# Kernel optimization log

Measured on AMD Instinct MI355X. Metric: run time of the kernel, lower is better.

The kernel has to match this reference:

```python
import jax, jax.numpy as jnp
import numpy as np

B, H, W, C, NH = 400, 14, 14, 768, 12
HD = C // NH  # 64


def setup_inputs() -> dict:
    key = jax.random.key(0)
    ks = jax.random.split(key, 6)
    s = 0.02
    return {
        "hidden_states": jax.random.normal(ks[0], (B, H, W, C), jnp.float32),
        "qkv_w": jax.random.normal(ks[1], (3 * C, C), jnp.float32) * s,
        "qkv_b": jnp.zeros((3 * C,), jnp.float32),
        "proj_w": jax.random.normal(ks[2], (C, C), jnp.float32) * s,
        "proj_b": jnp.zeros((C,), jnp.float32),
        "rel_pos_h": jax.random.normal(ks[3], (2 * H - 1, HD), jnp.float32) * s,
        "rel_pos_w": jax.random.normal(ks[4], (2 * W - 1, HD), jnp.float32) * s,
    }


def _get_rel_pos(q_size, k_size, rel_pos):
    # q_size == k_size and table already has 2*k-1 entries -> pure gather,
    # matching SamVisionAttention.get_rel_pos without interpolation.
    coords = jnp.arange(q_size)[:, None] - jnp.arange(k_size)[None, :] + (k_size - 1)
    return rel_pos[coords]  # (q, k, head_dim)


def reference(hidden_states, qkv_w, qkv_b, proj_w, proj_b, rel_pos_h, rel_pos_w):
    b, h, w, c = hidden_states.shape
    scale = HD ** -0.5
    # qkv projection: (b, h*w, 3c) -> (3, b, nh, hw, hd)
    qkv = hidden_states.reshape(b, h * w, c) @ qkv_w.T + qkv_b
    qkv = qkv.reshape(b, h * w, 3, NH, HD).transpose(2, 0, 3, 1, 4)
    q, k, v = qkv[0], qkv[1], qkv[2]
    # decomposed relative position bias (computed from UNSCALED q, as in SAM)
    Rh = _get_rel_pos(h, h, rel_pos_h)  # (h, h, hd)
    Rw = _get_rel_pos(w, w, rel_pos_w)  # (w, w, hd)
    qr = q.reshape(b, NH, h, w, HD)
    rel_h = jnp.einsum('bnhwc,hkc->bnhwk', qr, Rh)  # (b, nh, h, w, h)
    rel_w = jnp.einsum('bnhwc,wkc->bnhwk', qr, Rw)  # (b, nh, h, w, w)
    bias = (rel_h[..., :, None] + rel_w[..., None, :]).reshape(b, NH, h * w, h * w)
    # attention
    attn = jnp.einsum('bnqd,bnkd->bnqk', q, k) * scale + bias
    attn = jax.nn.softmax(attn, axis=-1)
    out = jnp.einsum('bnqk,bnkd->bnqd', attn, v)
    out = out.transpose(0, 2, 1, 3).reshape(b, h, w, c)
    return out @ proj_w.T + proj_b
```

## Files before the change

kernel.cpp:

```cpp
#include <hip/hip_runtime.h>
#include <hip/hip_bf16.h>

typedef __bf16 bfv8 __attribute__((ext_vector_type(8)));
typedef __bf16 bfv4 __attribute__((ext_vector_type(4)));
typedef float f32x4 __attribute__((ext_vector_type(4)));
typedef unsigned int u32x2 __attribute__((ext_vector_type(2)));
typedef unsigned short u16;
typedef unsigned int u32;

#define MT 78400

#define SBAR() __builtin_amdgcn_s_barrier()
#define VMCNT(n) asm volatile("s_waitcnt vmcnt(" #n ")" ::: "memory")

__device__ __forceinline__ u16 f2bf(float f) {
  u32 x = __float_as_uint(f);
  return (u16)((x + 0x7FFFu + ((x >> 16) & 1u)) >> 16);
}

__device__ __forceinline__ void gld16(const void* g, void* l) {
  __builtin_amdgcn_global_load_lds((const __attribute__((address_space(1))) void*)g,
                                   (__attribute__((address_space(3))) void*)l, 16, 0, 0);
}

__global__ __launch_bounds__(256) void cvt_f32_bf16(const float* __restrict__ src,
                                                    u16* __restrict__ dst, int n8) {
  int stride = gridDim.x * 256;
  for (int i = blockIdx.x * 256 + threadIdx.x; i < n8; i += stride) {
    const float4* s = (const float4*)(src + (long)i * 8);
    float4 a = s[0], b = s[1];
    u32 p0 = f2bf(a.x) | ((u32)f2bf(a.y) << 16);
    u32 p1 = f2bf(a.z) | ((u32)f2bf(a.w) << 16);
    u32 p2 = f2bf(b.x) | ((u32)f2bf(b.y) << 16);
    u32 p3 = f2bf(b.z) | ((u32)f2bf(b.w) << 16);
    uint4 o = {p0, p1, p2, p3};
    *(uint4*)(dst + (long)i * 8) = o;
  }
}

__global__ __launch_bounds__(256) void indk_init(u16* __restrict__ T) {
  int i = blockIdx.x * 256 + threadIdx.x;
  if (i < 208 * 40) {
    int k = i / 40, j = i - (i / 40) * 40;
    int hk = k / 14, wk = k - hk * 14;
    T[i] = (j == hk || j == 16 + wk) ? 0x3F80 : 0;
  }
}

__device__ __forceinline__ void gemm256_main(const u16* __restrict__ A, const u16* __restrict__ W,
                                             u16* SH, int m0, int n0, int tid,
                                             f32x4 (&acc)[8][4]) {
  const int lane = tid & 63;
  const int q15 = lane & 15, g = lane >> 4;
  const int wid = tid >> 6;
  const int wm = wid >> 2, wn = wid & 3;
  const int x0 = (g ^ (q15 & 7)) << 3;
  const int arow0 = wm * 128 + q15;
  const int brow0 = wn * 64 + q15;

  const int r0 = tid >> 3;
  const int gc0 = ((tid & 7) ^ (r0 & 7)) << 3;
  int ra00 = m0 + r0;       if (ra00 > MT - 1) ra00 = MT - 1;
  int ra10 = m0 + 64 + r0;  if (ra10 > MT - 1) ra10 = MT - 1;
  int ra01 = m0 + 128 + r0; if (ra01 > MT - 1) ra01 = MT - 1;
  int ra11 = m0 + 192 + r0; if (ra11 > MT - 1) ra11 = MT - 1;
  const u16* aS00 = A + (long)ra00 * 768 + gc0;
  const u16* aS10 = A + (long)ra10 * 768 + gc0;
  const u16* aS01 = A + (long)ra01 * 768 + gc0;
  const u16* aS11 = A + (long)ra11 * 768 + gc0;
  const u16* bS00 = W + (long)(n0 + r0) * 768 + gc0;
  const u16* bS10 = W + (long)(n0 + 64 + r0) * 768 + gc0;
  const u16* bS01 = W + (long)(n0 + 128 + r0) * 768 + gc0;
  const u16* bS11 = W + (long)(n0 + 192 + r0) * 768 + gc0;
  u16* dA = SH + tid * 8;
  u16* dB = dA + 16384;

  auto STGA = [&](int sl, const u16* p0, const u16* p1, int hoff, int kt) {
    u16* d = dA + sl * 32768 + hoff;
    gld16(p0 + kt * 64, d);
    gld16(p1 + kt * 64, d + 4096);
  };
  auto STGB = [&](int sl, const u16* p0, const u16* p1, int hoff, int kt) {
    u16* d = dB + sl * 32768 + hoff;
    gld16(p0 + kt * 64, d);
    gld16(p1 + kt * 64, d + 4096);
  };

  bfv8 b0[4], b1[4];
  bfv8 aX0[2], aX1[2], aY0[2], aY1[2];

  STGB(0, bS00, bS10, 0, 0); STGB(0, bS01, bS11, 8192, 0);
  STGA(0, aS00, aS10, 0, 0); STGA(0, aS01, aS11, 8192, 0);
  STGB(1, bS00, bS10, 0, 1); STGB(1, bS01, bS11, 8192, 1);
  STGA(1, aS00, aS10, 0, 1);
  VMCNT(4);
  SBAR();
  {
    const u16* Sb = SH + 16384;
#pragma unroll
    for (int ni = 0; ni < 4; ++ni) {
      const u16* bp = Sb + (brow0 + ni * 16) * 64;
      b0[ni] = *(const bfv8*)(bp + x0);
      b1[ni] = *(const bfv8*)(bp + (x0 ^ 32));
    }
#pragma unroll
    for (int m2 = 0; m2 < 2; ++m2) {
      const u16* ap = SH + (arow0 + m2 * 16) * 64;
      aX0[m2] = *(const bfv8*)(ap + x0);
      aX1[m2] = *(const bfv8*)(ap + (x0 ^ 32));
    }
  }

  for (int u = 0; u < 12; ++u) {
    const int sl = u & 1;
    const u16* Sa = SH + sl * 32768;
    const u16* San = SH + (sl ^ 1) * 32768;
    const u16* Sbn = San + 16384;
    const int kn1 = (u + 1 < 12) ? u + 1 : 11;
    const int kn2 = (u + 2 < 12) ? u + 2 : 11;

    __builtin_amdgcn_s_setprio(1);
#pragma unroll
    for (int m2 = 0; m2 < 2; ++m2)
#pragma unroll
      for (int ni = 0; ni < 4; ++ni)
        acc[m2][ni] = __builtin_amdgcn_mfma_f32_16x16x32_bf16(aX0[m2], b0[ni], acc[m2][ni], 0, 0, 0);
#pragma unroll
    for (int m2 = 0; m2 < 2; ++m2)
#pragma unroll
      for (int ni = 0; ni < 4; ++ni)
        acc[m2][ni] = __builtin_amdgcn_mfma_f32_16x16x32_bf16(aX1[m2], b1[ni], acc[m2][ni], 0, 0, 0);
    __builtin_amdgcn_s_setprio(0);
    SBAR();
#pragma unroll
    for (int m2 = 0; m2 < 2; ++m2) {
      const u16* ap = Sa + (arow0 + (2 + m2) * 16) * 64;
      aY0[m2] = *(const bfv8*)(ap + x0);
      aY1[m2] = *(const bfv8*)(ap + (x0 ^ 32));
    }
    STGA(sl ^ 1, aS01, aS11, 8192, kn1);

    __builtin_amdgcn_s_setprio(1);
#pragma unroll
    for (int m2 = 0; m2 < 2; ++m2)
#pragma unroll
      for (int ni = 0; ni < 4; ++ni)
        acc[2 + m2][ni] = __builtin_amdgcn_mfma_f32_16x16x32_bf16(aY0[m2], b0[ni], acc[2 + m2][ni], 0, 0, 0);
#pragma unroll
    for (int m2 = 0; m2 < 2; ++m2)
#pragma unroll
      for (int ni = 0; ni < 4; ++ni)
        acc[2 + m2][ni] = __builtin_amdgcn_mfma_f32_16x16x32_bf16(aY1[m2], b1[ni], acc[2 + m2][ni], 0, 0, 0);
    __builtin_amdgcn_s_setprio(0);
    SBAR();
#pragma unroll
    for (int m2 = 0; m2 < 2; ++m2) {
      const u16* ap = Sa + (arow0 + (4 + m2) * 16) * 64;
      aX0[m2] = *(const bfv8*)(ap + x0);
      aX1[m2] = *(const bfv8*)(ap + (x0 ^ 32));
    }
    STGB(sl, bS00, bS10, 0, kn2);

    __builtin_amdgcn_s_setprio(1);
#pragma unroll
    for (int m2 = 0; m2 < 2; ++m2)
#pragma unroll
      for (int ni = 0; ni < 4; ++ni)
        acc[4 + m2][ni] = __builtin_amdgcn_mfma_f32_16x16x32_bf16(aX0[m2], b0[ni], acc[4 + m2][ni], 0, 0, 0);
#pragma unroll
    for (int m2 = 0; m2 < 2; ++m2)
#pragma unroll
      for (int ni = 0; ni < 4; ++ni)
        acc[4 + m2][ni] = __builtin_amdgcn_mfma_f32_16x16x32_bf16(aX1[m2], b1[ni], acc[4 + m2][ni], 0, 0, 0);
    __builtin_amdgcn_s_setprio(0);
    SBAR();
#pragma unroll
    for (int m2 = 0; m2 < 2; ++m2) {
      const u16* ap = Sa + (arow0 + (6 + m2) * 16) * 64;
      aY0[m2] = *(const bfv8*)(ap + x0);
      aY1[m2] = *(const bfv8*)(ap + (x0 ^ 32));
    }
    STGB(sl, bS01, bS11, 8192, kn2);

    __builtin_amdgcn_s_setprio(1);
#pragma unroll
    for (int m2 = 0; m2 < 2; ++m2)
#pragma unroll
      for (int ni = 0; ni < 4; ++ni)
        acc[6 + m2][ni] = __builtin_amdgcn_mfma_f32_16x16x32_bf16(aY0[m2], b0[ni], acc[6 + m2][ni], 0, 0, 0);
#pragma unroll
    for (int m2 = 0; m2 < 2; ++m2)
#pragma unroll
      for (int ni = 0; ni < 4; ++ni)
        acc[6 + m2][ni] = __builtin_amdgcn_mfma_f32_16x16x32_bf16(aY1[m2], b1[ni], acc[6 + m2][ni], 0, 0, 0);
    __builtin_amdgcn_s_setprio(0);
    VMCNT(4);
    SBAR();
    if (u < 11) {
#pragma unroll
      for (int ni = 0; ni < 4; ++ni) {
        const u16* bp = Sbn + (brow0 + ni * 16) * 64;
        b0[ni] = *(const bfv8*)(bp + x0);
        b1[ni] = *(const bfv8*)(bp + (x0 ^ 32));
      }
#pragma unroll
      for (int m2 = 0; m2 < 2; ++m2) {
        const u16* ap = San + (arow0 + m2 * 16) * 64;
        aX0[m2] = *(const bfv8*)(ap + x0);
        aX1[m2] = *(const bfv8*)(ap + (x0 ^ 32));
      }
    }
    STGA(sl, aS00, aS10, 0, kn2);
  }
  VMCNT(0);
}

__global__ __launch_bounds__(512, 2) void qkv_gemm(const u16* __restrict__ A, const u16* __restrict__ W,
                                                   const float* __restrict__ bias,
                                                   u16* __restrict__ Qo, u16* __restrict__ Ko,
                                                   u16* __restrict__ Vo) {
  extern __shared__ u16 SH[];
  const int tid = threadIdx.x;
  const int orig = blockIdx.x;
  const int xcd = orig & 7, ii = orig >> 3;
  const int wg = (xcd < 3 ? xcd * 346 : 1038 + (xcd - 3) * 345) + ii;
  const int mt = wg / 9, nt = wg - mt * 9;
  const int m0 = mt * 256, n0 = nt * 256;

  f32x4 acc[8][4];
#pragma unroll
  for (int i = 0; i < 8; ++i)
#pragma unroll
    for (int j = 0; j < 4; ++j) acc[i][j] = (f32x4){0.f, 0.f, 0.f, 0.f};

  gemm256_main(A, W, SH, m0, n0, tid, acc);

  const int lane = tid & 63, q15 = lane & 15, g = lane >> 4;
  const int wid = tid >> 6, wm = wid >> 2, wn = wid & 3;
  __syncthreads();
  const int sel = nt / 3;
  u16* dst = (sel == 0) ? Qo : (sel == 1) ? Ko : Vo;
  const int ntr = nt - sel * 3;
  u16* Cs = SH;

#pragma unroll
  for (int h = 0; h < 2; ++h) {
    if (wm == h) {
#pragma unroll
      for (int ni = 0; ni < 4; ++ni) {
        int col = wn * 64 + ni * 16 + q15;
        float bb = bias[n0 + col];
#pragma unroll
        for (int mi = 0; mi < 8; ++mi)
#pragma unroll
          for (int r = 0; r < 4; ++r)
            Cs[(mi * 16 + g * 4 + r) * 264 + col] = f2bf(acc[mi][ni][r] + bb);
      }
    }
    __syncthreads();
#pragma unroll
    for (int j = 0; j < 8; ++j) {
      int idx = tid + 512 * j;
      int row = idx >> 5, cc = idx & 31;
      int m = m0 + h * 128 + row;
      if (m < MT) {
        int b = m / 196, s = m - b * 196;
        int nh = ntr * 4 + (cc >> 3);
        int hd0 = (cc & 7) * 8;
        uint4 v = *(const uint4*)(Cs + row * 264 + cc * 8);
        *(uint4*)(dst + (long)b * 150528 + (long)s * 64 + nh * 12544 + hd0) = v;
      }
    }
    if (h == 0) __syncthreads();
  }
}

__global__ __launch_bounds__(512, 2) void proj_gemm(const u16* __restrict__ A, const u16* __restrict__ W,
                                                    const float* __restrict__ bias,
                                                    float* __restrict__ out) {
  extern __shared__ u16 SH[];
  const int tid = threadIdx.x;
  const int orig = blockIdx.x;
  const int xcd = orig & 7, ii = orig >> 3;
  const int wg = (xcd < 1 ? xcd * 116 : 116 + (xcd - 1) * 115) + ii;
  const int mt = wg / 3, nt = wg - mt * 3;
  const int m0 = mt * 256, n0 = nt * 256;

  f32x4 acc[8][4];
#pragma unroll
  for (int i = 0; i < 8; ++i)
#pragma unroll
    for (int j = 0; j < 4; ++j) acc[i][j] = (f32x4){0.f, 0.f, 0.f, 0.f};

  gemm256_main(A, W, SH, m0, n0, tid, acc);

  const int lane = tid & 63, q15 = lane & 15, g = lane >> 4;
  const int wid = tid >> 6, wm = wid >> 2, wn = wid & 3;

#pragma unroll
  for (int ni = 0; ni < 4; ++ni) {
    int n = n0 + wn * 64 + ni * 16 + q15;
    float bb = bias[n];
#pragma unroll
    for (int mi = 0; mi < 8; ++mi)
#pragma unroll
      for (int r = 0; r < 4; ++r) {
        int m = m0 + wm * 128 + mi * 16 + g * 4 + r;
        if (m < MT) out[(long)m * 768 + n] = acc[mi][ni][r] + bb;
      }
  }
}

#define KLDS_OFF 0
#define VT_OFF   26624
#define TH_OFF   59392
#define TW_OFF   63280
#define AW_OFF   67168
#define SMEM_SZ  77408

__global__ __launch_bounds__(512, 2) void attn_kernel(const u16* __restrict__ Q, const u16* __restrict__ K,
                                                      const u16* __restrict__ V,
                                                      const float* __restrict__ rph, const float* __restrict__ rpw,
                                                      const u16* __restrict__ IndKg,
                                                      u16* __restrict__ AO) {
  extern __shared__ char smem[];
  u16* Klds = (u16*)(smem + KLDS_OFF);
  u16* VT = (u16*)(smem + VT_OFF);
  u16* TH = (u16*)(smem + TH_OFF);
  u16* TW = (u16*)(smem + TW_OFF);
  const int tid = threadIdx.x, lane = tid & 63, wid = tid >> 6;
  const int q15 = lane & 15, g = lane >> 4;
  const int bnh = blockIdx.x;
  const int b = bnh / 12, nh = bnh - b * 12;
  const u16* Qg = Q + bnh * 12544;
  const u16* Kg = K + bnh * 12544;
  const u16* Vg = V + bnh * 12544;
  u16* AWw = (u16*)(smem + AW_OFF) + wid * 16 * 40;

  for (int c = tid; c < 1568; c += 512) {
    int krow = c >> 3, part = c & 7;
    gld16(Kg + krow * 64 + ((part ^ (krow & 7)) << 3), Klds + c * 8);
  }
  for (int idx = tid; idx < 1792; idx += 512) {
    int k = idx >> 3, nb = idx & 7;
    u32 w0 = 0, w1 = 0, w2 = 0, w3 = 0;
    if (k < 196) {
      uint4 t = *(const uint4*)(Vg + k * 64 + nb * 8);
      w0 = t.x; w1 = t.y; w2 = t.z; w3 = t.w;
    }
    u32 wv[4] = {w0, w1, w2, w3};
#pragma unroll
    for (int j = 0; j < 8; j++) {
      int n = nb * 8 + j;
      u16 val = (u16)(wv[j >> 1] >> ((j & 1) * 16));
      int blk = (k >> 3) ^ (n & 7) ^ (n >> 3);
      VT[n * 256 + blk * 8 + (k & 7)] = val;
    }
  }
  for (int i = tid; i < 27 * 64; i += 512) {
    int r = i >> 6, cc = i & 63;
    TH[r * 72 + cc] = f2bf(rph[i]);
    TW[r * 72 + cc] = f2bf(rpw[i]);
  }
  __syncthreads();

  const int ksw = q15 & 7;
  const int ko0 = (g ^ ksw) << 3;
  const int ko1 = ((g + 4) ^ ksw) << 3;

  const f32x4 zero = {0.f, 0.f, 0.f, 0.f};
  for (int qt = wid; qt < 13; qt += 8) {
    const int q0 = qt * 16;
    int qrow = q0 + q15; if (qrow > 195) qrow = 195;
    bfv8 qf0 = *(const bfv8*)(Qg + qrow * 64 + g * 8);
    bfv8 qf1 = *(const bfv8*)(Qg + qrow * 64 + 32 + g * 8);

    int hq0 = q0 / 14, hq1 = (q0 + 15) / 14;
    int rha = hq0 + 13 - q15; rha = rha < 0 ? 0 : (rha > 26 ? 26 : rha);
    int rhb = hq1 + 13 - q15; rhb = rhb < 0 ? 0 : (rhb > 26 ? 26 : rhb);
    int rwa = q15;
    int rwb = 16 + q15; if (rwb > 26) rwb = 26;
    f32x4 c0h = zero, c1h = zero, c0w = zero, c1w = zero;
    {
      bfv8 t0 = *(const bfv8*)(TH + rha * 72 + g * 8);
      bfv8 t1 = *(const bfv8*)(TH + rha * 72 + 32 + g * 8);
      c0h = __builtin_amdgcn_mfma_f32_16x16x32_bf16(qf0, t0, c0h, 0, 0, 0);
      c0h = __builtin_amdgcn_mfma_f32_16x16x32_bf16(qf1, t1, c0h, 0, 0, 0);
      bfv8 t2 = *(const bfv8*)(TH + rhb * 72 + g * 8);
      bfv8 t3 = *(const bfv8*)(TH + rhb * 72 + 32 + g * 8);
      c1h = __builtin_amdgcn_mfma_f32_16x16x32_bf16(qf0, t2, c1h, 0, 0, 0);
      c1h = __builtin_amdgcn_mfma_f32_16x16x32_bf16(qf1, t3, c1h, 0, 0, 0);
      bfv8 u0 = *(const bfv8*)(TW + rwa * 72 + g * 8);
      bfv8 u1 = *(const bfv8*)(TW + rwa * 72 + 32 + g * 8);
      c0w = __builtin_amdgcn_mfma_f32_16x16x32_bf16(qf0, u0, c0w, 0, 0, 0);
      c0w = __builtin_amdgcn_mfma_f32_16x16x32_bf16(qf1, u1, c0w, 0, 0, 0);
      bfv8 u2 = *(const bfv8*)(TW + rwb * 72 + g * 8);
      bfv8 u3 = *(const bfv8*)(TW + rwb * 72 + 32 + g * 8);
      c1w = __builtin_amdgcn_mfma_f32_16x16x32_bf16(qf0, u2, c1w, 0, 0, 0);
      c1w = __builtin_amdgcn_mfma_f32_16x16x32_bf16(qf1, u3, c1w, 0, 0, 0);
    }

#pragma unroll
    for (int r = 0; r < 4; r++) {
      int row = g * 4 + r;
      int qq = q0 + row;
      int hqr = qq / 14;
      int wq_r = qq - hqr * 14;
      if (q15 < 10) AWw[row * 40 + 30 + q15] = 0;
      float rh = ((hqr == hq1) ? c1h[r] : c0h[r]) * 8.0f;
      AWw[row * 40 + q15] = (q15 <= 13) ? f2bf(rh) : (u16)0;
      int w0p = wq_r + 13 - q15;
      if (w0p >= 0 && w0p <= 13) AWw[row * 40 + 16 + w0p] = f2bf(c0w[r] * 8.0f);
      int w1p = wq_r - 3 - q15;
      if (w1p >= 0 && w1p <= 13) AWw[row * 40 + 16 + w1p] = f2bf(c1w[r] * 8.0f);
    }
    bfv8 qaug = *(const bfv8*)(AWw + q15 * 40 + g * 8);

    f32x4 o[4] = {zero, zero, zero, zero};
    float den = 0.f;
#pragma unroll
    for (int t = 0; t < 13; t++) {
      const u16* kr = Klds + (t * 16 + q15) * 64;
      bfv8 kb0 = *(const bfv8*)(kr + ko0);
      bfv8 kb1 = *(const bfv8*)(kr + ko1);
      bfv8 ib = *(const bfv8*)(IndKg + (t * 16 + q15) * 40 + g * 8);
      __builtin_amdgcn_s_setprio(1);
      f32x4 a0 = __builtin_amdgcn_mfma_f32_16x16x32_bf16(ib, qaug, zero, 0, 0, 0);
      f32x4 a1 = __builtin_amdgcn_mfma_f32_16x16x32_bf16(kb0, qf0, a0, 0, 0, 0);
      f32x4 st = __builtin_amdgcn_mfma_f32_16x16x32_bf16(kb1, qf1, a1, 0, 0, 0);
      __builtin_amdgcn_s_setprio(0);
      float p0 = (t == 12 && g > 0) ? 0.f : exp2f(st[0] * 0.18033688f - 5.7707802f);
      float p1 = (t == 12 && g > 0) ? 0.f : exp2f(st[1] * 0.18033688f - 5.7707802f);
      float p2 = (t == 12 && g > 0) ? 0.f : exp2f(st[2] * 0.18033688f - 5.7707802f);
      float p3 = (t == 12 && g > 0) ? 0.f : exp2f(st[3] * 0.18033688f - 5.7707802f);
      den += (p0 + p1) + (p2 + p3);
      u32 lo, hi;
      asm("v_cvt_pk_bf16_f32 %0, %1, %2" : "=v"(lo) : "v"(p0), "v"(p1));
      asm("v_cvt_pk_bf16_f32 %0, %1, %2" : "=v"(hi) : "v"(p2), "v"(p3));
      u32x2 w; w.x = lo; w.y = hi;
      bfv4 pa = __builtin_bit_cast(bfv4, w);
      const int kblk = 2 * t + (g >> 1);
      const int koff = (g & 1) * 4;
      __builtin_amdgcn_s_setprio(1);
#pragma unroll
      for (int nt_ = 0; nt_ < 4; nt_++) {
        int n = nt_ * 16 + q15;
        int blk = (kblk ^ (n & 7) ^ (n >> 3));
        bfv4 vb = *(const bfv4*)(VT + n * 256 + blk * 8 + koff);
        asm("v_mfma_f32_16x16x16_bf16 %0, %1, %2, %0" : "+v"(o[nt_]) : "v"(pa), "v"(vb));
      }
      __builtin_amdgcn_s_setprio(0);
    }
    den += __shfl_xor(den, 16);
    den += __shfl_xor(den, 32);
    float inv = 1.0f / den;
    float invr[4];
#pragma unroll
    for (int r = 0; r < 4; r++) invr[r] = __shfl(inv, g * 4 + r);

#pragma unroll
    for (int nt_ = 0; nt_ < 4; nt_++)
#pragma unroll
      for (int r = 0; r < 4; r++) {
        int s_ = q0 + g * 4 + r;
        if (s_ < 196) AO[((long)(b * 196 + s_)) * 768 + nh * 64 + nt_ * 16 + q15] = f2bf(o[nt_][r] * invr[r]);
      }
  }
}

#define GEMM_LDS 131072

extern "C" void kernel_launch(void* const* d_in, const int* in_sizes, int n_in,
                              void* d_out, int out_size, void* d_ws, size_t ws_size,
                              hipStream_t stream) {
  const float* hs = (const float*)d_in[0];
  const float* qkvw = (const float*)d_in[1];
  const float* qkvb = (const float*)d_in[2];
  const float* projw = (const float*)d_in[3];
  const float* projb = (const float*)d_in[4];
  const float* rph = (const float*)d_in[5];
  const float* rpw = (const float*)d_in[6];

  char* ws = (char*)d_ws;
  u16* Xb = (u16*)ws;
  u16* Wq = (u16*)(ws + 120422400);
  u16* Wp = (u16*)(ws + 123961344);
  u16* Qb = (u16*)(ws + 125140992);
  u16* Kb = (u16*)(ws + 245563392);
  u16* Vb = (u16*)(ws + 365985792);
  u16* AO = Xb;
  u16* IndKg = Wq;

  cvt_f32_bf16<<<2048, 256, 0, stream>>>(hs, Xb, 7526400);
  cvt_f32_bf16<<<864, 256, 0, stream>>>(qkvw, Wq, 221184);
  cvt_f32_bf16<<<288, 256, 0, stream>>>(projw, Wp, 73728);

  hipFuncSetAttribute((const void*)qkv_gemm, hipFuncAttributeMaxDynamicSharedMemorySize, GEMM_LDS);
  qkv_gemm<<<2763, 512, GEMM_LDS, stream>>>(Xb, Wq, qkvb, Qb, Kb, Vb);

  indk_init<<<33, 256, 0, stream>>>(IndKg);

  hipFuncSetAttribute((const void*)attn_kernel, hipFuncAttributeMaxDynamicSharedMemorySize, SMEM_SZ);
  attn_kernel<<<4800, 512, SMEM_SZ, stream>>>(Qb, Kb, Vb, rph, rpw, IndKg, AO);

  hipFuncSetAttribute((const void*)proj_gemm, hipFuncAttributeMaxDynamicSharedMemorySize, GEMM_LDS);
  proj_gemm<<<921, 512, GEMM_LDS, stream>>>(AO, Wp, projb, (float*)d_out);
}
```

Before: 837.9 us.

## Shrink GEMM tiles to 128x256 with 3-stage K32 LDS pipeline

Replaces the 256x256 GEMM mainloop (K=64 steps, double-buffered, 128KB LDS) used by the QKV and projection GEMMs with a 128x256 tile that steps K in chunks of 32 through a triple-buffered LDS ring using 72KB. The grids roughly double, so more workgroups are available to fill the CUs and the tail is finer, and the smaller LDS footprint allows two workgroups per CU. In exchange each tile does half the MFMA work per operand load, which lowers arithmetic intensity and doubles the number of barriers per K.

```diff
diff --git a/kernel.cpp b/kernel.cpp
--- a/kernel.cpp
+++ b/kernel.cpp
@@ -47,170 +47,67 @@
   }
 }
 
-__device__ __forceinline__ void gemm256_main(const u16* __restrict__ A, const u16* __restrict__ W,
+__device__ __forceinline__ void gemm128_main(const u16* __restrict__ A, const u16* __restrict__ W,
                                              u16* SH, int m0, int n0, int tid,
-                                             f32x4 (&acc)[8][4]) {
+                                             f32x4 (&acc)[4][4]) {
   const int lane = tid & 63;
   const int q15 = lane & 15, g = lane >> 4;
   const int wid = tid >> 6;
   const int wm = wid >> 2, wn = wid & 3;
-  const int x0 = (g ^ (q15 & 7)) << 3;
-  const int arow0 = wm * 128 + q15;
+  const int xa = ((g ^ (q15 & 3)) << 3);
+  const int arow0 = wm * 64 + q15;
   const int brow0 = wn * 64 + q15;
 
-  const int r0 = tid >> 3;
-  const int gc0 = ((tid & 7) ^ (r0 & 7)) << 3;
-  int ra00 = m0 + r0;       if (ra00 > MT - 1) ra00 = MT - 1;
-  int ra10 = m0 + 64 + r0;  if (ra10 > MT - 1) ra10 = MT - 1;
-  int ra01 = m0 + 128 + r0; if (ra01 > MT - 1) ra01 = MT - 1;
-  int ra11 = m0 + 192 + r0; if (ra11 > MT - 1) ra11 = MT - 1;
-  const u16* aS00 = A + (long)ra00 * 768 + gc0;
-  const u16* aS10 = A + (long)ra10 * 768 + gc0;
-  const u16* aS01 = A + (long)ra01 * 768 + gc0;
-  const u16* aS11 = A + (long)ra11 * 768 + gc0;
-  const u16* bS00 = W + (long)(n0 + r0) * 768 + gc0;
-  const u16* bS10 = W + (long)(n0 + 64 + r0) * 768 + gc0;
-  const u16* bS01 = W + (long)(n0 + 128 + r0) * 768 + gc0;
-  const u16* bS11 = W + (long)(n0 + 192 + r0) * 768 + gc0;
+  const int rA = tid >> 2;
+  const int gcA = (((tid & 3) ^ (rA & 3)) << 3);
+  int ra = m0 + rA; if (ra > MT - 1) ra = MT - 1;
+  const u16* aP = A + (long)ra * 768 + gcA;
+  const u16* bP0 = W + (long)(n0 + rA) * 768 + gcA;
+  const u16* bP1 = W + (long)(n0 + 128 + rA) * 768 + gcA;
   u16* dA = SH + tid * 8;
-  u16* dB = dA + 16384;
-
-  auto STGA = [&](int sl, const u16* p0, const u16* p1, int hoff, int kt) {
-    u16* d = dA + sl * 32768 + hoff;
-    gld16(p0 + kt * 64, d);
-    gld16(p1 + kt * 64, d + 4096);
-  };
-  auto STGB = [&](int sl, const u16* p0, const u16* p1, int hoff, int kt) {
-    u16* d = dB + sl * 32768 + hoff;
-    gld16(p0 + kt * 64, d);
-    gld16(p1 + kt * 64, d + 4096);
-  };
-
-  bfv8 b0[4], b1[4];
-  bfv8 aX0[2], aX1[2], aY0[2], aY1[2];
-
-  STGB(0, bS00, bS10, 0, 0); STGB(0, bS01, bS11, 8192, 0);
-  STGA(0, aS00, aS10, 0, 0); STGA(0, aS01, aS11, 8192, 0);
-  STGB(1, bS00, bS10, 0, 1); STGB(1, bS01, bS11, 8192, 1);
-  STGA(1, aS00, aS10, 0, 1);
-  VMCNT(4);
+  u16* dB = SH + 4096 + tid * 8;
+
+  bfv8 af[4], bf[4];
+
+  gld16(aP + 0, dA);            gld16(bP0 + 0, dB);            gld16(bP1 + 0, dB + 4096);
+  gld16(aP + 32, dA + 12288);   gld16(bP0 + 32, dB + 12288);   gld16(bP1 + 32, dB + 16384);
+  VMCNT(3);
   SBAR();
-  {
-    const u16* Sb = SH + 16384;
-#pragma unroll
-    for (int ni = 0; ni < 4; ++ni) {
-      const u16* bp = Sb + (brow0 + ni * 16) * 64;
-      b0[ni] = *(const bfv8*)(bp + x0);
-      b1[ni] = *(const bfv8*)(bp + (x0 ^ 32));
-    }
-#pragma unroll
-    for (int m2 = 0; m2 < 2; ++m2) {
-      const u16* ap = SH + (arow0 + m2 * 16) * 64;
-      aX0[m2] = *(const bfv8*)(ap + x0);
-      aX1[m2] = *(const bfv8*)(ap + (x0 ^ 32));
-    }
-  }
-
-  for (int u = 0; u < 12; ++u) {
-    const int sl = u & 1;
-    const u16* Sa = SH + sl * 32768;
-    const u16* San = SH + (sl ^ 1) * 32768;
-    const u16* Sbn = San + 16384;
-    const int kn1 = (u + 1 < 12) ? u + 1 : 11;
-    const int kn2 = (u + 2 < 12) ? u + 2 : 11;
-
+#pragma unroll
+  for (int mi = 0; mi < 4; ++mi) af[mi] = *(const bfv8*)(SH + (arow0 + mi * 16) * 32 + xa);
+#pragma unroll
+  for (int ni = 0; ni < 4; ++ni) bf[ni] = *(const bfv8*)(SH + 4096 + (brow0 + ni * 16) * 32 + xa);
+
+  int so2 = 24576;
+  int so1 = 12288;
+  for (int u = 0; u < 24; ++u) {
+    const int kn = (u + 2 < 24) ? u + 2 : 23;
     __builtin_amdgcn_s_setprio(1);
 #pragma unroll
-    for (int m2 = 0; m2 < 2; ++m2)
+    for (int mi = 0; mi < 4; ++mi)
 #pragma unroll
       for (int ni = 0; ni < 4; ++ni)
-        acc[m2][ni] = __builtin_amdgcn_mfma_f32_16x16x32_bf16(aX0[m2], b0[ni], acc[m2][ni], 0, 0, 0);
-#pragma unroll
-    for (int m2 = 0; m2 < 2; ++m2)
-#pragma unroll
-      for (int ni = 0; ni < 4; ++ni)
-        acc[m2][ni] = __builtin_amdgcn_mfma_f32_16x16x32_bf16(aX1[m2], b1[ni], acc[m2][ni], 0, 0, 0);
+        acc[mi][ni] = __builtin_amdgcn_mfma_f32_16x16x32_bf16(af[mi], bf[ni], acc[mi][ni], 0, 0, 0);
     __builtin_amdgcn_s_setprio(0);
+    {
+      u16* da = dA + so2;
+      u16* db = dB + so2;
+      gld16(aP + kn * 32, da);
+      gld16(bP0 + kn * 32, db);
+      gld16(bP1 + kn * 32, db + 4096);
+    }
+    VMCNT(3);
     SBAR();
-#pragma unroll
-    for (int m2 = 0; m2 < 2; ++m2) {
-      const u16* ap = Sa + (arow0 + (2 + m2) * 16) * 64;
-      aY0[m2] = *(const bfv8*)(ap + x0);
-      aY1[m2] = *(const bfv8*)(ap + (x0 ^ 32));
-    }
-    STGA(sl ^ 1, aS01, aS11, 8192, kn1);
-
-    __builtin_amdgcn_s_setprio(1);
-#pragma unroll
-    for (int m2 = 0; m2 < 2; ++m2)
-#pragma unroll
-      for (int ni = 0; ni < 4; ++ni)
-        acc[2 + m2][ni] = __builtin_amdgcn_mfma_f32_16x16x32_bf16(aY0[m2], b0[ni], acc[2 + m2][ni], 0, 0, 0);
-#pragma unroll
-    for (int m2 = 0; m2 < 2; ++m2)
-#pragma unroll
-      for (int ni = 0; ni < 4; ++ni)
-        acc[2 + m2][ni] = __builtin_amdgcn_mfma_f32_16x16x32_bf16(aY1[m2], b1[ni], acc[2 + m2][ni], 0, 0, 0);
-    __builtin_amdgcn_s_setprio(0);
-    SBAR();
-#pragma unroll
-    for (int m2 = 0; m2 < 2; ++m2) {
-      const u16* ap = Sa + (arow0 + (4 + m2) * 16) * 64;
-      aX0[m2] = *(const bfv8*)(ap + x0);
-      aX1[m2] = *(const bfv8*)(ap + (x0 ^ 32));
-    }
-    STGB(sl, bS00, bS10, 0, kn2);
-
-    __builtin_amdgcn_s_setprio(1);
-#pragma unroll
-    for (int m2 = 0; m2 < 2; ++m2)
-#pragma unroll
-      for (int ni = 0; ni < 4; ++ni)
-        acc[4 + m2][ni] = __builtin_amdgcn_mfma_f32_16x16x32_bf16(aX0[m2], b0[ni], acc[4 + m2][ni], 0, 0, 0);
-#pragma unroll
-    for (int m2 = 0; m2 < 2; ++m2)
-#pragma unroll
-      for (int ni = 0; ni < 4; ++ni)
-        acc[4 + m2][ni] = __builtin_amdgcn_mfma_f32_16x16x32_bf16(aX1[m2], b1[ni], acc[4 + m2][ni], 0, 0, 0);
-    __builtin_amdgcn_s_setprio(0);
-    SBAR();
-#pragma unroll
-    for (int m2 = 0; m2 < 2; ++m2) {
-      const u16* ap = Sa + (arow0 + (6 + m2) * 16) * 64;
-      aY0[m2] = *(const bfv8*)(ap + x0);
-      aY1[m2] = *(const bfv8*)(ap + (x0 ^ 32));
-    }
-    STGB(sl, bS01, bS11, 8192, kn2);
-
-    __builtin_amdgcn_s_setprio(1);
-#pragma unroll
-    for (int m2 = 0; m2 < 2; ++m2)
-#pragma unroll
-      for (int ni = 0; ni < 4; ++ni)
-        acc[6 + m2][ni] = __builtin_amdgcn_mfma_f32_16x16x32_bf16(aY0[m2], b0[ni], acc[6 + m2][ni], 0, 0, 0);
-#pragma unroll
-    for (int m2 = 0; m2 < 2; ++m2)
-#pragma unroll
-      for (int ni = 0; ni < 4; ++ni)
-        acc[6 + m2][ni] = __builtin_amdgcn_mfma_f32_16x16x32_bf16(aY1[m2], b1[ni], acc[6 + m2][ni], 0, 0, 0);
-    __builtin_amdgcn_s_setprio(0);
-    VMCNT(4);
-    SBAR();
-    if (u < 11) {
-#pragma unroll
-      for (int ni = 0; ni < 4; ++ni) {
-        const u16* bp = Sbn + (brow0 + ni * 16) * 64;
-        b0[ni] = *(const bfv8*)(bp + x0);
-        b1[ni] = *(const bfv8*)(bp + (x0 ^ 32));
-      }
-#pragma unroll
-      for (int m2 = 0; m2 < 2; ++m2) {
-        const u16* ap = San + (arow0 + m2 * 16) * 64;
-        aX0[m2] = *(const bfv8*)(ap + x0);
-        aX1[m2] = *(const bfv8*)(ap + (x0 ^ 32));
-      }
-    }
-    STGA(sl, aS00, aS10, 0, kn2);
+    if (u < 23) {
+      const u16* Sa = SH + so1;
+      const u16* Sb = Sa + 4096;
+#pragma unroll
+      for (int mi = 0; mi < 4; ++mi) af[mi] = *(const bfv8*)(Sa + (arow0 + mi * 16) * 32 + xa);
+#pragma unroll
+      for (int ni = 0; ni < 4; ++ni) bf[ni] = *(const bfv8*)(Sb + (brow0 + ni * 16) * 32 + xa);
+    }
+    so2 = (so2 == 24576) ? 0 : so2 + 12288;
+    so1 = (so1 == 24576) ? 0 : so1 + 12288;
   }
   VMCNT(0);
 }
@@ -223,17 +120,17 @@
   const int tid = threadIdx.x;
   const int orig = blockIdx.x;
   const int xcd = orig & 7, ii = orig >> 3;
-  const int wg = (xcd < 3 ? xcd * 346 : 1038 + (xcd - 3) * 345) + ii;
+  const int wg = (xcd < 5 ? xcd * 690 : 3450 + (xcd - 5) * 689) + ii;
   const int mt = wg / 9, nt = wg - mt * 9;
-  const int m0 = mt * 256, n0 = nt * 256;
-
-  f32x4 acc[8][4];
-#pragma unroll
-  for (int i = 0; i < 8; ++i)
+  const int m0 = mt * 128, n0 = nt * 256;
+
+  f32x4 acc[4][4];
+#pragma unroll
+  for (int i = 0; i < 4; ++i)
 #pragma unroll
     for (int j = 0; j < 4; ++j) acc[i][j] = (f32x4){0.f, 0.f, 0.f, 0.f};
 
-  gemm256_main(A, W, SH, m0, n0, tid, acc);
+  gemm128_main(A, W, SH, m0, n0, tid, acc);
 
   const int lane = tid & 63, q15 = lane & 15, g = lane >> 4;
   const int wid = tid >> 6, wm = wid >> 2, wn = wid & 3;
@@ -244,34 +141,28 @@
   u16* Cs = SH;
 
 #pragma unroll
-  for (int h = 0; h < 2; ++h) {
-    if (wm == h) {
-#pragma unroll
-      for (int ni = 0; ni < 4; ++ni) {
-        int col = wn * 64 + ni * 16 + q15;
-        float bb = bias[n0 + col];
-#pragma unroll
-        for (int mi = 0; mi < 8; ++mi)
-#pragma unroll
-          for (int r = 0; r < 4; ++r)
-            Cs[(mi * 16 + g * 4 + r) * 264 + col] = f2bf(acc[mi][ni][r] + bb);
-      }
-    }
-    __syncthreads();
-#pragma unroll
-    for (int j = 0; j < 8; ++j) {
-      int idx = tid + 512 * j;
-      int row = idx >> 5, cc = idx & 31;
-      int m = m0 + h * 128 + row;
-      if (m < MT) {
-        int b = m / 196, s = m - b * 196;
-        int nh = ntr * 4 + (cc >> 3);
-        int hd0 = (cc & 7) * 8;
-        uint4 v = *(const uint4*)(Cs + row * 264 + cc * 8);
-        *(uint4*)(dst + (long)b * 150528 + (long)s * 64 + nh * 12544 + hd0) = v;
-      }
-    }
-    if (h == 0) __syncthreads();
+  for (int ni = 0; ni < 4; ++ni) {
+    int col = wn * 64 + ni * 16 + q15;
+    float bb = bias[n0 + col];
+#pragma unroll
+    for (int mi = 0; mi < 4; ++mi)
+#pragma unroll
+      for (int r = 0; r < 4; ++r)
+        Cs[(wm * 64 + mi * 16 + g * 4 + r) * 264 + col] = f2bf(acc[mi][ni][r] + bb);
+  }
+  __syncthreads();
+#pragma unroll
+  for (int j = 0; j < 8; ++j) {
+    int idx = tid + 512 * j;
+    int row = idx >> 5, cc = idx & 31;
+    int m = m0 + row;
+    if (m < MT) {
+      int b = m / 196, s = m - b * 196;
+      int nh = ntr * 4 + (cc >> 3);
+      int hd0 = (cc & 7) * 8;
+      uint4 v = *(const uint4*)(Cs + row * 264 + cc * 8);
+      *(uint4*)(dst + (long)b * 150528 + (long)s * 64 + nh * 12544 + hd0) = v;
+    }
   }
 }
 
@@ -282,17 +173,17 @@
   const int tid = threadIdx.x;
   const int orig = blockIdx.x;
   const int xcd = orig & 7, ii = orig >> 3;
-  const int wg = (xcd < 1 ? xcd * 116 : 116 + (xcd - 1) * 115) + ii;
+  const int wg = (xcd < 7 ? xcd * 230 : 1610 + (xcd - 7) * 229) + ii;
   const int mt = wg / 3, nt = wg - mt * 3;
-  const int m0 = mt * 256, n0 = nt * 256;
-
-  f32x4 acc[8][4];
-#pragma unroll
-  for (int i = 0; i < 8; ++i)
+  const int m0 = mt * 128, n0 = nt * 256;
+
+  f32x4 acc[4][4];
+#pragma unroll
+  for (int i = 0; i < 4; ++i)
 #pragma unroll
     for (int j = 0; j < 4; ++j) acc[i][j] = (f32x4){0.f, 0.f, 0.f, 0.f};
 
-  gemm256_main(A, W, SH, m0, n0, tid, acc);
+  gemm128_main(A, W, SH, m0, n0, tid, acc);
 
   const int lane = tid & 63, q15 = lane & 15, g = lane >> 4;
   const int wid = tid >> 6, wm = wid >> 2, wn = wid & 3;
@@ -302,10 +193,10 @@
     int n = n0 + wn * 64 + ni * 16 + q15;
     float bb = bias[n];
 #pragma unroll
-    for (int mi = 0; mi < 8; ++mi)
+    for (int mi = 0; mi < 4; ++mi)
 #pragma unroll
       for (int r = 0; r < 4; ++r) {
-        int m = m0 + wm * 128 + mi * 16 + g * 4 + r;
+        int m = m0 + wm * 64 + mi * 16 + g * 4 + r;
         if (m < MT) out[(long)m * 768 + n] = acc[mi][ni][r] + bb;
       }
   }
@@ -468,7 +359,8 @@
   }
 }
 
-#define GEMM_LDS 131072
+#define QKV_LDS 73728
+#define PROJ_LDS 73728
 
 extern "C" void kernel_launch(void* const* d_in, const int* in_sizes, int n_in,
                               void* d_out, int out_size, void* d_ws, size_t ws_size,
@@ -495,14 +387,14 @@
   cvt_f32_bf16<<<864, 256, 0, stream>>>(qkvw, Wq, 221184);
   cvt_f32_bf16<<<288, 256, 0, stream>>>(projw, Wp, 73728);
 
-  hipFuncSetAttribute((const void*)qkv_gemm, hipFuncAttributeMaxDynamicSharedMemorySize, GEMM_LDS);
-  qkv_gemm<<<2763, 512, GEMM_LDS, stream>>>(Xb, Wq, qkvb, Qb, Kb, Vb);
+  hipFuncSetAttribute((const void*)qkv_gemm, hipFuncAttributeMaxDynamicSharedMemorySize, QKV_LDS);
+  qkv_gemm<<<5517, 512, QKV_LDS, stream>>>(Xb, Wq, qkvb, Qb, Kb, Vb);
 
   indk_init<<<33, 256, 0, stream>>>(IndKg);
 
   hipFuncSetAttribute((const void*)attn_kernel, hipFuncAttributeMaxDynamicSharedMemorySize, SMEM_SZ);
   attn_kernel<<<4800, 512, SMEM_SZ, stream>>>(Qb, Kb, Vb, rph, rpw, IndKg, AO);
 
-  hipFuncSetAttribute((const void*)proj_gemm, hipFuncAttributeMaxDynamicSharedMemorySize, GEMM_LDS);
-  proj_gemm<<<921, 512, GEMM_LDS, stream>>>(AO, Wp, projb, (float*)d_out);
-}
+  hipFuncSetAttribute((const void*)proj_gemm, hipFuncAttributeMaxDynamicSharedMemorySize, PROJ_LDS);
+  proj_gemm<<<1839, 512, PROJ_LDS, stream>>>(AO, Wp, projb, (float*)d_out);
+}
```

After: 903.3 us. 1.08x slower.
